# Optimization experiments

Measured on AMD Instinct MI355X. Metric: run time of the kernel, lower is better.

Reference implementation:

```python
import jax, jax.numpy as jnp
import numpy as np

B, N, D, H, DH, HID, CONT, FF = 4, 384, 256, 4, 64, 64, 6, 2
DIST, DIR, ROLE, HOPD, EDGE, SP, DEG, CELL, SAME = 9, 10, 10, 4, 5, 6, 18, 65, 3
SCALE = DH ** -0.5

def _gelu(t):
    return jax.nn.gelu(t, approximate=False)

def _ln(x, g, b, eps=1e-5):
    m = x.mean(-1, keepdims=True)
    v = ((x - m) ** 2).mean(-1, keepdims=True)
    return (x - m) / jnp.sqrt(v + eps) * g + b

def setup_inputs() -> dict:
    key = jax.random.key(0)
    ks = iter(jax.random.split(key, 64))
    nrm = lambda shape, s=0.02: jax.random.normal(next(ks), shape, jnp.float32) * s
    ri = lambda hi, shape: jax.random.randint(next(ks), shape, 0, hi, jnp.int32)
    x = jax.random.normal(next(ks), (B, N, D), jnp.float32)
    cont = jax.random.normal(next(ks), (B, N, N, CONT), jnp.float32)
    pair_mask = jax.random.bernoulli(next(ks), 0.25, (B, N, N)) | jnp.eye(N, dtype=bool)[None]
    valid_mask = jax.random.bernoulli(next(ks), 0.9, (B, N)).at[:, 0].set(True)
    z = lambda *s: jnp.zeros(s, jnp.float32)
    o = lambda *s: jnp.ones(s, jnp.float32)
    return dict(
        x=x, pair_mask=pair_mask, valid_mask=valid_mask, continuous_features=cont,
        distance_bucket=ri(DIST, (B, N, N)), direction_bucket=ri(DIR, (B, N, N)),
        role_pair_id=ri(ROLE, (B, N, N)), hop_delta=ri(HOPD, (B, N, N)),
        edge_type=ri(EDGE, (B, N, N)), shortest_path_bucket=ri(SP, (B, N, N)),
        same_cell_type=ri(SAME, (B, N, N)), degree_ids=ri(DEG, (B, N)), cell_type_ids=ri(CELL, (B, N)),
        Wq=nrm((H * DH, D)), Wk=nrm((H * DH, D)), Wv=nrm((H * DH, D)),
        Wo=nrm((D, H * DH)), bo=z(D),
        cm_W1=nrm((HID, CONT)), cm_b1=z(HID), cm_W2=nrm((HID, HID)), cm_b2=z(HID),
        E_dist=nrm((DIST, HID)), E_dir=nrm((DIR, HID)), E_role=nrm((ROLE, HID)),
        E_hop=nrm((HOPD, HID)), E_edge=nrm((EDGE, HID)), E_sp=nrm((SP, HID)),
        E_deg=nrm((DEG, HID)).at[0].set(0.0), E_cell=nrm((CELL, HID)).at[0].set(0.0),
        E_same=nrm((SAME, HID)),
        bias_ln_g=o(HID), bias_ln_b=z(HID), bias_W=nrm((H, HID)), bias_b=z(H),
        ln1_g=o(D), ln1_b=z(D), ln2_g=o(D), ln2_b=z(D),
        ff_W1=nrm((D * FF * 2, D)), ff_b1=z(D * FF * 2), ff_W2=nrm((D, D * FF)), ff_b2=z(D),
    )

def reference(x, pair_mask, valid_mask, continuous_features, distance_bucket, direction_bucket,
              role_pair_id, hop_delta, edge_type, shortest_path_bucket, same_cell_type,
              degree_ids, cell_type_ids, Wq, Wk, Wv, Wo, bo, cm_W1, cm_b1, cm_W2, cm_b2,
              E_dist, E_dir, E_role, E_hop, E_edge, E_sp, E_deg, E_cell, E_same,
              bias_ln_g, bias_ln_b, bias_W, bias_b, ln1_g, ln1_b, ln2_g, ln2_b,
              ff_W1, ff_b1, ff_W2, ff_b2):
    # --- pairwise structural bias: [B,N,N,HID] pair repr -> [B,H,N,N] bias ---
    pr = _gelu(continuous_features @ cm_W1.T + cm_b1) @ cm_W2.T + cm_b2
    pr = pr + E_dist[distance_bucket] + E_dir[direction_bucket] + E_role[role_pair_id]
    pr = pr + E_hop[hop_delta] + E_edge[edge_type] + E_sp[shortest_path_bucket] + E_same[same_cell_type]
    deg = E_deg[degree_ids]            # [B,N,HID]
    cel = E_cell[cell_type_ids]        # [B,N,HID]
    pr = pr + deg[:, :, None, :] + deg[:, None, :, :] + cel[:, :, None, :] + cel[:, None, :, :]
    bias = _gelu(_ln(pr, bias_ln_g, bias_ln_b)) @ bias_W.T + bias_b   # [B,N,N,H]
    bias = bias * pair_mask[..., None].astype(bias.dtype)
    bias = jnp.transpose(bias, (0, 3, 1, 2))                          # [B,H,N,N]
    # --- attention ---
    xn = _ln(x, ln1_g, ln1_b)
    q = (xn @ Wq.T).reshape(B, N, H, DH).transpose(0, 2, 1, 3)
    k = (xn @ Wk.T).reshape(B, N, H, DH).transpose(0, 2, 1, 3)
    v = (xn @ Wv.T).reshape(B, N, H, DH).transpose(0, 2, 1, 3)
    logits = jnp.einsum('bhid,bhjd->bhij', q, k) * SCALE + bias
    eye = jnp.eye(N, dtype=bool)
    safe = pair_mask | ((~valid_mask)[:, :, None] & eye[None])
    logits = jnp.where(safe[:, None], logits, -jnp.finfo(logits.dtype).max)
    attn = jax.nn.softmax(logits, axis=-1)
    attn = attn * pair_mask[:, None].astype(attn.dtype)
    attn = attn / jnp.maximum(attn.sum(-1, keepdims=True), 1e-6)
    out = jnp.einsum('bhij,bhjd->bhid', attn, v).transpose(0, 2, 1, 3).reshape(B, N, H * DH)
    x1 = x + (out @ Wo.T + bo)
    # --- GEGLU feed-forward ---
    h = _ln(x1, ln2_g, ln2_b) @ ff_W1.T + ff_b1
    a, g = h[..., :D * FF], h[..., D * FF:]
    x_out = x1 + ((a * _gelu(g)) @ ff_W2.T + ff_b2)
    return (x_out, attn, bias)
```

## Files before the change

### kernel.cpp

```cpp
#include <hip/hip_runtime.h>
#include <hip/hip_bf16.h>
#include <float.h>

#define Bz   4
#define Nn   384
#define Dd   256
#define Hh   4
#define DHh  64
#define NSQ  (384*384)
#define NEG_MAX (-3.40282346638528859812e+38f)

typedef __attribute__((ext_vector_type(8))) short short8;
typedef __attribute__((ext_vector_type(4))) float f32x4;
typedef unsigned short ushort_t;

__device__ __forceinline__ float gelu_f(float x){
  const float y = __builtin_fabsf(x) * 0.70710678118654752f;
  const float t = __builtin_amdgcn_rcpf(fmaf(0.3275911f, y, 1.0f));
  float poly = fmaf(1.061405429f, t, -1.453152027f);
  poly = fmaf(poly, t, 1.421413741f);
  poly = fmaf(poly, t, -0.284496736f);
  poly = fmaf(poly, t, 0.254829592f);
  poly *= t;
  const float e = __expf(-y * y);
  const float erfa = fmaf(-poly, e, 1.0f);
  const float er = __builtin_copysignf(erfa, x);
  return 0.5f * x * (1.0f + er);
}
__device__ __forceinline__ float wsum(float v){
  #pragma unroll
  for (int o = 32; o > 0; o >>= 1) v += __shfl_xor(v, o, 64);
  return v;
}
__device__ __forceinline__ float4 ld4(const float* p){ return *(const float4*)p; }
__device__ __forceinline__ f32x4 ldv4(const float* p){ return *(const f32x4*)p; }

__device__ __forceinline__ ushort_t f2bfu(float f){
  union { float f; unsigned u; } v; v.f = f;
  unsigned r = v.u + 0x7FFFu + ((v.u >> 16) & 1u);
  return (ushort_t)(r >> 16);
}
__device__ __forceinline__ short f2bf(float f){ return (short)f2bfu(f); }
__device__ __forceinline__ float bfe2f(ushort_t u){
  union { unsigned u; float f; } v; v.u = ((unsigned)u) << 16; return v.f;
}
__device__ __forceinline__ void addbf(f32x4& a, f32x4& b, short8 v){
  a[0] += bfe2f((ushort_t)v[0]); a[1] += bfe2f((ushort_t)v[1]);
  a[2] += bfe2f((ushort_t)v[2]); a[3] += bfe2f((ushort_t)v[3]);
  b[0] += bfe2f((ushort_t)v[4]); b[1] += bfe2f((ushort_t)v[5]);
  b[2] += bfe2f((ushort_t)v[6]); b[3] += bfe2f((ushort_t)v[7]);
}

__global__ __launch_bounds__(256) void prep_kernel(
    const int* __restrict__ dgk, const int* __restrict__ ctk,
    const float* __restrict__ Edg, const float* __restrict__ Ec,
    const float* __restrict__ b2,
    const float* __restrict__ W1, const float* __restrict__ b1,
    const float* __restrict__ W2,
    const float* __restrict__ Ed, const float* __restrict__ Edi,
    const float* __restrict__ Er, const float* __restrict__ Eh,
    const float* __restrict__ Ee, const float* __restrict__ Esp,
    const float* __restrict__ Es,
    const float* __restrict__ Wq, const float* __restrict__ Wk,
    const float* __restrict__ Wv, const float* __restrict__ Wo,
    const float* __restrict__ ffW1, const float* __restrict__ ffW2,
    const int* __restrict__ dbk, const int* __restrict__ drk,
    const int* __restrict__ rpk, const int* __restrict__ hdk,
    const int* __restrict__ etk, const int* __restrict__ spk,
    const int* __restrict__ sck, const int* __restrict__ pm,
    const float* __restrict__ cont,
    ushort_t* __restrict__ dcP, ushort_t* __restrict__ dcbP,
    ushort_t* __restrict__ w1bf, ushort_t* __restrict__ w2bf,
    ushort_t* __restrict__ EddP, ushort_t* __restrict__ ErsP,
    ushort_t* __restrict__ EhesP,
    ushort_t* __restrict__ wqB, ushort_t* __restrict__ wkB,
    ushort_t* __restrict__ wvB, ushort_t* __restrict__ woB,
    ushort_t* __restrict__ ffW1B, ushort_t* __restrict__ ffW2B,
    ushort_t* __restrict__ contP)
{
  const int idx = blockIdx.x * 256 + threadIdx.x;
  if (idx < 24576) {
    const int row = idx >> 4;
    const int q   = (idx & 15) << 2;
    const int pos = ((q >> 2) & 3) * 16 + (q >> 4) * 4;
    const float4 a = ld4(Edg + (dgk[row] << 6) + q);
    const float4 b = ld4(Ec  + (ctk[row] << 6) + q);
    const float4 bb4 = ld4(b2 + q);
    ushort4 o, o2;
    o.x = f2bfu(a.x + b.x); o.y = f2bfu(a.y + b.y);
    o.z = f2bfu(a.z + b.z); o.w = f2bfu(a.w + b.w);
    o2.x = f2bfu(a.x + b.x + bb4.x); o2.y = f2bfu(a.y + b.y + bb4.y);
    o2.z = f2bfu(a.z + b.z + bb4.z); o2.w = f2bfu(a.w + b.w + bb4.w);
    *(ushort4*)(dcP  + row * 64 + pos) = o;
    *(ushort4*)(dcbP + row * 64 + pos) = o2;
  } else if (idx < 26624) {
    const int t = idx - 24576;
    const int c = t >> 5, k2 = (t & 31) << 1;
    w2bf[c * 64 + k2]     = f2bfu(W2[c * 64 + k2]);
    w2bf[c * 64 + k2 + 1] = f2bfu(W2[c * 64 + k2 + 1]);
  } else if (idx < 26688) {
    const int k = idx - 26624;
    #pragma unroll
    for (int d = 0; d < 6; ++d) w1bf[k * 8 + d] = f2bfu(W1[k * 6 + d]);
    w1bf[k * 8 + 6] = f2bfu(b1[k]);
    w1bf[k * 8 + 7] = 0;
  } else if (idx < 28128) {
    const int t = idx - 26688;
    const int row = t >> 4, q = (t & 15) << 2;
    const int pos = ((q >> 2) & 3) * 16 + (q >> 4) * 4;
    const int d = row / 10, r = row - d * 10;
    const float4 a = ld4(Ed + (d << 6) + q);
    const float4 b = ld4(Edi + (r << 6) + q);
    ushort4 o;
    o.x = f2bfu(a.x + b.x); o.y = f2bfu(a.y + b.y);
    o.z = f2bfu(a.z + b.z); o.w = f2bfu(a.w + b.w);
    *(ushort4*)(EddP + row * 64 + pos) = o;
  } else if (idx < 29088) {
    const int t = idx - 28128;
    const int row = t >> 4, q = (t & 15) << 2;
    const int pos = ((q >> 2) & 3) * 16 + (q >> 4) * 4;
    const int ro = row / 6, s = row - ro * 6;
    const float4 a = ld4(Er + (ro << 6) + q);
    const float4 b = ld4(Esp + (s << 6) + q);
    ushort4 o;
    o.x = f2bfu(a.x + b.x); o.y = f2bfu(a.y + b.y);
    o.z = f2bfu(a.z + b.z); o.w = f2bfu(a.w + b.w);
    *(ushort4*)(ErsP + row * 64 + pos) = o;
  } else if (idx < 30048) {
    const int t = idx - 29088;
    const int row = t >> 4, q = (t & 15) << 2;
    const int pos = ((q >> 2) & 3) * 16 + (q >> 4) * 4;
    const int h = row / 15, rem = row - h * 15;
    const int e = rem / 3, sm = rem - e * 3;
    const float4 a = ld4(Eh + (h << 6) + q);
    const float4 b = ld4(Ee + (e << 6) + q);
    const float4 c = ld4(Es + (sm << 6) + q);
    ushort4 o;
    o.x = f2bfu(a.x + b.x + c.x); o.y = f2bfu(a.y + b.y + c.y);
    o.z = f2bfu(a.z + b.z + c.z); o.w = f2bfu(a.w + b.w + c.w);
    *(ushort4*)(EhesP + row * 64 + pos) = o;
  } else if (idx < 193888) {
    const int t = idx - 30048;
    const float* src; ushort_t* dst; int e;
    if (t < 16384)      { src = Wq;   dst = wqB;   e = t << 2; }
    else if (t < 32768) { src = Wk;   dst = wkB;   e = (t - 16384) << 2; }
    else if (t < 49152) { src = Wv;   dst = wvB;   e = (t - 32768) << 2; }
    else if (t < 65536) { src = Wo;   dst = woB;   e = (t - 49152) << 2; }
    else if (t < 131072){ src = ffW1; dst = ffW1B; e = (t - 65536) << 2; }
    else                { src = ffW2; dst = ffW2B; e = (t - 131072) << 2; }
    const float4 v = ld4(src + e);
    ushort4 o;
    o.x = f2bfu(v.x); o.y = f2bfu(v.y); o.z = f2bfu(v.z); o.w = f2bfu(v.w);
    *(ushort4*)(dst + e) = o;
  } else if (idx < 193888 + Bz * Nn * Nn) {
    const int p = idx - 193888;
    const float* cp = cont + (size_t)p * 6;
    short8 r;
    r[0] = f2bf(cp[0]); r[1] = f2bf(cp[1]); r[2] = f2bf(cp[2]);
    r[3] = f2bf(cp[3]); r[4] = f2bf(cp[4]); r[5] = f2bf(cp[5]);
    const unsigned iv = (unsigned)(dbk[p] * 10 + drk[p])
                      | ((unsigned)(rpk[p] * 6 + spk[p]) << 7)
                      | ((unsigned)((hdk[p] * 5 + etk[p]) * 3 + sck[p]) << 13)
                      | ((pm[p] ? 1u : 0u) << 19);
    r[6] = (short)(iv & 0xffffu);
    r[7] = (short)(iv >> 16);
    *(short8*)(contP + (size_t)p * 8) = r;
  }
}

__global__ __launch_bounds__(256, 3) void pair_kernel(
    const ushort_t* __restrict__ contP,
    const ushort_t* __restrict__ w1bf, const ushort_t* __restrict__ w2bf,
    const ushort_t* __restrict__ EddP, const ushort_t* __restrict__ ErsP,
    const ushort_t* __restrict__ EhesP,
    const float* __restrict__ lng, const float* __restrict__ lnb,
    const float* __restrict__ bW, const float* __restrict__ bb,
    const ushort_t* __restrict__ dcP, const ushort_t* __restrict__ dcbP,
    float* __restrict__ biasOut)
{
  const int tid  = threadIdx.x;
  const int lane = tid & 63;
  const int l15  = lane & 15, lg = lane >> 4;
  const int wid  = blockIdx.x * 4 + (tid >> 6);
  const int rowU = __builtin_amdgcn_readfirstlane(wid / 6);
  const int jb   = wid - rowU * 6;
  const int b    = rowU / Nn;
  const int i    = rowU - b * Nn;
  const int j0   = jb * 64 + l15;
  const size_t pbase = (size_t)rowU * Nn + j0;
  const int colOff = lg << 2;

  const short8 rec0 = *(const short8*)(contP + (pbase + 0) * 8);
  const short8 rec1 = *(const short8*)(contP + (pbase + 16) * 8);
  const short8 rec2 = *(const short8*)(contP + (pbase + 32) * 8);
  const short8 rec3 = *(const short8*)(contP + (pbase + 48) * 8);
  asm volatile("" :: "v"(rec0), "v"(rec1), "v"(rec2), "v"(rec3));
  const unsigned ix0 = (unsigned)(ushort_t)rec0[6] | ((unsigned)(ushort_t)rec0[7] << 16);
  const unsigned ix1 = (unsigned)(ushort_t)rec1[6] | ((unsigned)(ushort_t)rec1[7] << 16);
  const unsigned ix2 = (unsigned)(ushort_t)rec2[6] | ((unsigned)(ushort_t)rec2[7] << 16);
  const unsigned ix3 = (unsigned)(ushort_t)rec3[6] | ((unsigned)(ushort_t)rec3[7] << 16);
  const float c00 = bfe2f((ushort_t)rec0[0]), c01 = bfe2f((ushort_t)rec0[1]),
              c02 = bfe2f((ushort_t)rec0[2]), c03 = bfe2f((ushort_t)rec0[3]),
              c04 = bfe2f((ushort_t)rec0[4]), c05 = bfe2f((ushort_t)rec0[5]);
  const float c10 = bfe2f((ushort_t)rec1[0]), c11 = bfe2f((ushort_t)rec1[1]),
              c12 = bfe2f((ushort_t)rec1[2]), c13 = bfe2f((ushort_t)rec1[3]),
              c14 = bfe2f((ushort_t)rec1[4]), c15 = bfe2f((ushort_t)rec1[5]);
  const float c20 = bfe2f((ushort_t)rec2[0]), c21 = bfe2f((ushort_t)rec2[1]),
              c22 = bfe2f((ushort_t)rec2[2]), c23 = bfe2f((ushort_t)rec2[3]),
              c24 = bfe2f((ushort_t)rec2[4]), c25 = bfe2f((ushort_t)rec2[5]);
  const float c30 = bfe2f((ushort_t)rec3[0]), c31 = bfe2f((ushort_t)rec3[1]),
              c32 = bfe2f((ushort_t)rec3[2]), c33 = bfe2f((ushort_t)rec3[3]),
              c34 = bfe2f((ushort_t)rec3[4]), c35 = bfe2f((ushort_t)rec3[5]);

  short8 b0a, b0b, b1a, b1b, b2a, b2b, b3a, b3b;
#define H1ROW(R, JJ, D0, D1, D2, D3) { \
    const float w0 = bfe2f((ushort_t)R[0]), w1 = bfe2f((ushort_t)R[1]), \
                w2 = bfe2f((ushort_t)R[2]), w3 = bfe2f((ushort_t)R[3]), \
                w4 = bfe2f((ushort_t)R[4]), w5 = bfe2f((ushort_t)R[5]), \
                w6 = bfe2f((ushort_t)R[6]); \
    float s0 = w6, s1 = w6, s2 = w6, s3 = w6; \
    s0 = fmaf(w0, c00, s0); s0 = fmaf(w1, c01, s0); s0 = fmaf(w2, c02, s0); \
    s0 = fmaf(w3, c03, s0); s0 = fmaf(w4, c04, s0); s0 = fmaf(w5, c05, s0); \
    s1 = fmaf(w0, c10, s1); s1 = fmaf(w1, c11, s1); s1 = fmaf(w2, c12, s1); \
    s1 = fmaf(w3, c13, s1); s1 = fmaf(w4, c14, s1); s1 = fmaf(w5, c15, s1); \
    s2 = fmaf(w0, c20, s2); s2 = fmaf(w1, c21, s2); s2 = fmaf(w2, c22, s2); \
    s2 = fmaf(w3, c23, s2); s2 = fmaf(w4, c24, s2); s2 = fmaf(w5, c25, s2); \
    s3 = fmaf(w0, c30, s3); s3 = fmaf(w1, c31, s3); s3 = fmaf(w2, c32, s3); \
    s3 = fmaf(w3, c33, s3); s3 = fmaf(w4, c34, s3); s3 = fmaf(w5, c35, s3); \
    D0[JJ] = f2bf(gelu_f(s0)); D1[JJ] = f2bf(gelu_f(s1)); \
    D2[JJ] = f2bf(gelu_f(s2)); D3[JJ] = f2bf(gelu_f(s3)); }
  {
    const ushort_t* wb_ = w1bf + ((lg << 3) << 3);
    const short8 r0 = *(const short8*)(wb_ +  0);
    const short8 r1 = *(const short8*)(wb_ +  8);
    const short8 r2 = *(const short8*)(wb_ + 16);
    const short8 r3 = *(const short8*)(wb_ + 24);
    const short8 r4 = *(const short8*)(wb_ + 32);
    const short8 r5 = *(const short8*)(wb_ + 40);
    const short8 r6 = *(const short8*)(wb_ + 48);
    const short8 r7 = *(const short8*)(wb_ + 56);
    asm volatile("" :: "v"(r0), "v"(r1), "v"(r2), "v"(r3),
                       "v"(r4), "v"(r5), "v"(r6), "v"(r7));
    H1ROW(r0, 0, b0a, b1a, b2a, b3a) H1ROW(r1, 1, b0a, b1a, b2a, b3a)
    H1ROW(r2, 2, b0a, b1a, b2a, b3a) H1ROW(r3, 3, b0a, b1a, b2a, b3a)
    H1ROW(r4, 4, b0a, b1a, b2a, b3a) H1ROW(r5, 5, b0a, b1a, b2a, b3a)
    H1ROW(r6, 6, b0a, b1a, b2a, b3a) H1ROW(r7, 7, b0a, b1a, b2a, b3a)
  }
  {
    const ushort_t* wb_ = w1bf + ((32 + (lg << 3)) << 3);
    const short8 r0 = *(const short8*)(wb_ +  0);
    const short8 r1 = *(const short8*)(wb_ +  8);
    const short8 r2 = *(const short8*)(wb_ + 16);
    const short8 r3 = *(const short8*)(wb_ + 24);
    const short8 r4 = *(const short8*)(wb_ + 32);
    const short8 r5 = *(const short8*)(wb_ + 40);
    const short8 r6 = *(const short8*)(wb_ + 48);
    const short8 r7 = *(const short8*)(wb_ + 56);
    asm volatile("" :: "v"(r0), "v"(r1), "v"(r2), "v"(r3),
                       "v"(r4), "v"(r5), "v"(r6), "v"(r7));
    H1ROW(r0, 0, b0b, b1b, b2b, b3b) H1ROW(r1, 1, b0b, b1b, b2b, b3b)
    H1ROW(r2, 2, b0b, b1b, b2b, b3b) H1ROW(r3, 3, b0b, b1b, b2b, b3b)
    H1ROW(r4, 4, b0b, b1b, b2b, b3b) H1ROW(r5, 5, b0b, b1b, b2b, b3b)
    H1ROW(r6, 6, b0b, b1b, b2b, b3b) H1ROW(r7, 7, b0b, b1b, b2b, b3b)
  }
#undef H1ROW

  const ushort_t* wbase = w2bf + (size_t)l15 * 64 + (lg << 3);
  const short8 wa0 = *(const short8*)(wbase);
  const short8 wc0 = *(const short8*)(wbase + 32);
  const short8 wa1 = *(const short8*)(wbase + 16 * 64);
  const short8 wc1 = *(const short8*)(wbase + 16 * 64 + 32);
  const short8 wa2 = *(const short8*)(wbase + 32 * 64);
  const short8 wc2 = *(const short8*)(wbase + 32 * 64 + 32);
  const short8 wa3 = *(const short8*)(wbase + 48 * 64);
  const short8 wc3 = *(const short8*)(wbase + 48 * 64 + 32);
  asm volatile("" :: "v"(wa0), "v"(wc0), "v"(wa1), "v"(wc1),
                     "v"(wa2), "v"(wc2), "v"(wa3), "v"(wc3));
  f32x4 acc0[4] = {}, acc1[4] = {}, acc2[4] = {}, acc3[4] = {};
#define MM(ACC, BA, BB) \
  ACC[0] = __builtin_amdgcn_mfma_f32_16x16x32_bf16(wa0, BA, ACC[0], 0, 0, 0); \
  ACC[0] = __builtin_amdgcn_mfma_f32_16x16x32_bf16(wc0, BB, ACC[0], 0, 0, 0); \
  ACC[1] = __builtin_amdgcn_mfma_f32_16x16x32_bf16(wa1, BA, ACC[1], 0, 0, 0); \
  ACC[1] = __builtin_amdgcn_mfma_f32_16x16x32_bf16(wc1, BB, ACC[1], 0, 0, 0); \
  ACC[2] = __builtin_amdgcn_mfma_f32_16x16x32_bf16(wa2, BA, ACC[2], 0, 0, 0); \
  ACC[2] = __builtin_amdgcn_mfma_f32_16x16x32_bf16(wc2, BB, ACC[2], 0, 0, 0); \
  ACC[3] = __builtin_amdgcn_mfma_f32_16x16x32_bf16(wa3, BA, ACC[3], 0, 0, 0); \
  ACC[3] = __builtin_amdgcn_mfma_f32_16x16x32_bf16(wc3, BB, ACC[3], 0, 0, 0);
  MM(acc0, b0a, b0b) MM(acc1, b1a, b1b) MM(acc2, b2a, b2b) MM(acc3, b3a, b3b)
#undef MM

#define GATHER(ACC, IX, JOFF) { \
    const int xdd  = ((IX) & 127) << 6; \
    const int xrs  = (((IX) >> 7) & 63) << 6; \
    const int xhes = (((IX) >> 13) & 63) << 6; \
    const ushort_t* ep = EddP  + xdd  + (lg << 4); \
    const ushort_t* rp = ErsP  + xrs  + (lg << 4); \
    const ushort_t* hp = EhesP + xhes + (lg << 4); \
    const ushort_t* jp = dcP + (((size_t)(b * Nn + j0 + (JOFF))) << 6) + (lg << 4); \
    const short8 e0 = *(const short8*)ep,       e1 = *(const short8*)(ep + 8); \
    const short8 r0 = *(const short8*)rp,       r1 = *(const short8*)(rp + 8); \
    const short8 h0 = *(const short8*)hp,       h1 = *(const short8*)(hp + 8); \
    const short8 jv0 = *(const short8*)jp,      jv1 = *(const short8*)(jp + 8); \
    asm volatile("" :: "v"(e0), "v"(e1), "v"(r0), "v"(r1), \
                       "v"(h0), "v"(h1), "v"(jv0), "v"(jv1)); \
    addbf(ACC[0], ACC[1], e0);  addbf(ACC[2], ACC[3], e1); \
    addbf(ACC[0], ACC[1], r0);  addbf(ACC[2], ACC[3], r1); \
    addbf(ACC[0], ACC[1], h0);  addbf(ACC[2], ACC[3], h1); \
    addbf(ACC[0], ACC[1], jv0); addbf(ACC[2], ACC[3], jv1); }
  GATHER(acc0, ix0, 0)
  GATHER(acc1, ix1, 16)
  GATHER(acc2, ix2, 32)
  GATHER(acc3, ix3, 48)
#undef GATHER
  {
    const ushort_t* up = dcbP + (((size_t)rowU) << 6) + (lg << 4);
    const short8 u0 = *(const short8*)up, u1 = *(const short8*)(up + 8);
    f32x4 du0, du1, du2, du3;
    #pragma unroll
    for (int r = 0; r < 4; ++r) {
      du0[r] = bfe2f((ushort_t)u0[r]);     du1[r] = bfe2f((ushort_t)u0[4 + r]);
      du2[r] = bfe2f((ushort_t)u1[r]);     du3[r] = bfe2f((ushort_t)u1[4 + r]);
    }
    acc0[0] += du0; acc0[1] += du1; acc0[2] += du2; acc0[3] += du3;
    acc1[0] += du0; acc1[1] += du1; acc1[2] += du2; acc1[3] += du3;
    acc2[0] += du0; acc2[1] += du1; acc2[2] += du2; acc2[3] += du3;
    acc3[0] += du0; acc3[1] += du1; acc3[2] += du2; acc3[3] += du3;
  }

  float mean0, inv0, mean1, inv1, mean2, inv2, mean3, inv3;
#define STATS(ACC, MEAN, INV) { \
    float sum = 0.f, sq = 0.f; \
    _Pragma("unroll") \
    for (int mt = 0; mt < 4; ++mt) \
      _Pragma("unroll") \
      for (int r = 0; r < 4; ++r) { \
        const float v = ACC[mt][r]; sum += v; sq = fmaf(v, v, sq); } \
    sum += __shfl_xor(sum, 16, 64); sum += __shfl_xor(sum, 32, 64); \
    sq  += __shfl_xor(sq,  16, 64); sq  += __shfl_xor(sq,  32, 64); \
    MEAN = sum * (1.f / 64.f); \
    INV  = rsqrtf(sq * (1.f / 64.f) - MEAN * MEAN + 1e-5f); }
  STATS(acc0, mean0, inv0) STATS(acc1, mean1, inv1)
  STATS(acc2, mean2, inv2) STATS(acc3, mean3, inv3)
#undef STATS

  float h00 = 0.f, h01 = 0.f, h02 = 0.f, h03 = 0.f;
  float h10 = 0.f, h11 = 0.f, h12 = 0.f, h13 = 0.f;
  float h20 = 0.f, h21 = 0.f, h22 = 0.f, h23 = 0.f;
  float h30 = 0.f, h31 = 0.f, h32 = 0.f, h33 = 0.f;
  #pragma unroll
  for (int mt = 0; mt < 4; ++mt) {
    const int c0i = (mt << 4) + colOff;
    const f32x4 g4 = ldv4(lng + c0i);
    const f32x4 b4 = ldv4(lnb + c0i);
    const f32x4 w0 = ldv4(bW + c0i);
    const f32x4 w1_ = ldv4(bW + 64 + c0i);
    const f32x4 w2_ = ldv4(bW + 128 + c0i);
    const f32x4 w3_ = ldv4(bW + 192 + c0i);
    asm volatile("" :: "v"(g4), "v"(b4), "v"(w0), "v"(w1_), "v"(w2_), "v"(w3_));
    #pragma unroll
    for (int r = 0; r < 4; ++r) {
      float g;
      g = gelu_f((acc0[mt][r] - mean0) * inv0 * g4[r] + b4[r]);
      h00 = fmaf(w0[r], g, h00); h01 = fmaf(w1_[r], g, h01);
      h02 = fmaf(w2_[r], g, h02); h03 = fmaf(w3_[r], g, h03);
      g = gelu_f((acc1[mt][r] - mean1) * inv1 * g4[r] + b4[r]);
      h10 = fmaf(w0[r], g, h10); h11 = fmaf(w1_[r], g, h11);
      h12 = fmaf(w2_[r], g, h12); h13 = fmaf(w3_[r], g, h13);
      g = gelu_f((acc2[mt][r] - mean2) * inv2 * g4[r] + b4[r]);
      h20 = fmaf(w0[r], g, h20); h21 = fmaf(w1_[r], g, h21);
      h22 = fmaf(w2_[r], g, h22); h23 = fmaf(w3_[r], g, h23);
      g = gelu_f((acc3[mt][r] - mean3) * inv3 * g4[r] + b4[r]);
      h30 = fmaf(w0[r], g, h30); h31 = fmaf(w1_[r], g, h31);
      h32 = fmaf(w2_[r], g, h32); h33 = fmaf(w3_[r], g, h33);
    }
  }
#define RED(H) H += __shfl_xor(H, 16, 64); H += __shfl_xor(H, 32, 64);
  RED(h00) RED(h01) RED(h02) RED(h03)
  RED(h10) RED(h11) RED(h12) RED(h13)
  RED(h20) RED(h21) RED(h22) RED(h23)
  RED(h30) RED(h31) RED(h32) RED(h33)
#undef RED

  const float bbl = bb[lg];
  const float bh0 = ((lg == 0) ? h00 : (lg == 1) ? h01 : (lg == 2) ? h02 : h03) + bbl;
  const float bh1 = ((lg == 0) ? h10 : (lg == 1) ? h11 : (lg == 2) ? h12 : h13) + bbl;
  const float bh2 = ((lg == 0) ? h20 : (lg == 1) ? h21 : (lg == 2) ? h22 : h23) + bbl;
  const float bh3 = ((lg == 0) ? h30 : (lg == 1) ? h31 : (lg == 2) ? h32 : h33) + bbl;
  const size_t base = (size_t)b * (Hh * NSQ) + (size_t)lg * NSQ + (size_t)i * Nn;
  biasOut[base + j0]      = bh0 * (((ix0 >> 19) & 1) ? 1.f : 0.f);
  biasOut[base + j0 + 16] = bh1 * (((ix1 >> 19) & 1) ? 1.f : 0.f);
  biasOut[base + j0 + 32] = bh2 * (((ix2 >> 19) & 1) ? 1.f : 0.f);
  biasOut[base + j0 + 48] = bh3 * (((ix3 >> 19) & 1) ? 1.f : 0.f);
}

__global__ __launch_bounds__(256) void ln_kernel(
    const float* __restrict__ x, const float* __restrict__ g,
    const float* __restrict__ bta, ushort_t* __restrict__ o)
{
  const int row  = blockIdx.x * 4 + (threadIdx.x >> 6);
  const int lane = threadIdx.x & 63;
  const float4 v = *(const float4*)(x + (size_t)row * Dd + lane * 4);
  float s = v.x + v.y + v.z + v.w;
  s = wsum(s);
  const float m = s * (1.f / 256.f);
  const float dx = v.x - m, dy = v.y - m, dz = v.z - m, dw = v.w - m;
  float q = dx*dx + dy*dy + dz*dz + dw*dw;
  q = wsum(q);
  const float inv = rsqrtf(q * (1.f / 256.f) + 1e-5f);
  const int d = lane * 4;
  const float4 gg = *(const float4*)(g + d);
  const float4 bb = *(const float4*)(bta + d);
  ushort4 out;
  out.x = f2bfu(dx * inv * gg.x + bb.x);
  out.y = f2bfu(dy * inv * gg.y + bb.y);
  out.z = f2bfu(dz * inv * gg.z + bb.z);
  out.w = f2bfu(dw * inv * gg.w + bb.w);
  *(ushort4*)(o + (size_t)row * Dd + d) = out;
}

__global__ __launch_bounds__(256) void qkv_kernel(
    const ushort_t* __restrict__ xnb,
    const ushort_t* __restrict__ wqB, const ushort_t* __restrict__ wkB,
    const ushort_t* __restrict__ wvB,
    ushort_t* __restrict__ qbB, ushort_t* __restrict__ kbB,
    ushort_t* __restrict__ vbT)
{
  const int tid = threadIdx.x;
  const int lane = tid & 63;
  const int w   = tid >> 6;
  const int l15 = lane & 15, lg = lane >> 4;
  const int m0 = blockIdx.y * 64 + w * 16;
  const int n0 = blockIdx.x * 64;
  const int z  = blockIdx.z;
  const ushort_t* Bb = (z == 0) ? wqB : (z == 1) ? wkB : wvB;

  f32x4 acc[4] = {};
  const ushort_t* pa = xnb + (size_t)(m0 + l15) * Dd + lg * 8;
  for (int k0 = 0; k0 < Dd; k0 += 32) {
    const short8 af = *(const short8*)(pa + k0);
    #pragma unroll
    for (int nt = 0; nt < 4; ++nt) {
      const short8 bf = *(const short8*)(Bb +
          (size_t)(n0 + nt * 16 + l15) * Dd + k0 + lg * 8);
      acc[nt] = __builtin_amdgcn_mfma_f32_16x16x32_bf16(af, bf, acc[nt], 0, 0, 0);
    }
  }
  if (z < 2) {
    ushort_t* Cb = (z == 0) ? qbB : kbB;
    #pragma unroll
    for (int nt = 0; nt < 4; ++nt)
      #pragma unroll
      for (int r = 0; r < 4; ++r)
        Cb[(size_t)(m0 + lg * 4 + r) * Dd + n0 + nt * 16 + l15] = f2bfu(acc[nt][r]);
  } else {
    const int m = m0 + (lg << 2);
    const int b = m / Nn, tok = m - b * Nn;
    #pragma unroll
    for (int nt = 0; nt < 4; ++nt) {
      const int n = n0 + nt * 16 + l15;
      const int h = n >> 6, dh = n & 63;
      ushort4 s4;
      s4.x = f2bfu(acc[nt][0]); s4.y = f2bfu(acc[nt][1]);
      s4.z = f2bfu(acc[nt][2]); s4.w = f2bfu(acc[nt][3]);
      *(ushort4*)(vbT + ((size_t)((b * 4 + h) * 64 + dh)) * Nn + tok) = s4;
    }
  }
}

template<int MODE>
__global__ __launch_bounds__(256) void gemm2(
    const ushort_t* __restrict__ A16, const float* __restrict__ A32, int lda,
    const ushort_t* __restrict__ Bm, int ldb,
    float* __restrict__ Cc, int ldc,
    const float* __restrict__ bias,
    const float* __restrict__ res, int ldr,
    int K,
    const float* __restrict__ biasT, const int* __restrict__ pmask,
    const int* __restrict__ valid)
{
  const int tid = threadIdx.x;
  const int lane = tid & 63;
  const int w   = tid >> 6;
  const int l15 = lane & 15, lg = lane >> 4;
  const int m0 = blockIdx.y * 64 + w * 16;
  const int n0 = blockIdx.x * 64;

  const ushort_t* Ab = A16; const ushort_t* Bb = Bm; float* Cb = Cc;
  const float* biasTb = biasT; const int* pmb = pmask; const int* vlb = valid;
  if (MODE == 1) {
    const int bz = blockIdx.z;
    const int b = bz >> 2, h = bz & 3;
    Ab = A16 + (size_t)b * Nn * Dd + h * DHh;
    Bb = Bm  + (size_t)b * Nn * Dd + h * DHh;
    Cb = Cc + (size_t)bz * NSQ;
    biasTb = biasT + (size_t)bz * NSQ;
    pmb = pmask + (size_t)b * NSQ;
    vlb = valid + b * Nn;
  }

  f32x4 acc[4] = {};
  const ushort_t* pa16 = Ab + (size_t)(m0 + l15) * lda + lg * 8;
  const float* pa32 = (MODE == 3) ? (A32 + (size_t)(m0 + l15) * lda + lg * 8) : nullptr;

  for (int k0 = 0; k0 < K; k0 += 32) {
    short8 af;
    if (MODE == 3) {
      const float4 a0 = ld4(pa32 + k0);
      const float4 a1 = ld4(pa32 + k0 + 4);
      const float4 g0 = ld4(pa32 + 512 + k0);
      const float4 g1 = ld4(pa32 + 512 + k0 + 4);
      af[0] = f2bf(a0.x * gelu_f(g0.x)); af[1] = f2bf(a0.y * gelu_f(g0.y));
      af[2] = f2bf(a0.z * gelu_f(g0.z)); af[3] = f2bf(a0.w * gelu_f(g0.w));
      af[4] = f2bf(a1.x * gelu_f(g1.x)); af[5] = f2bf(a1.y * gelu_f(g1.y));
      af[6] = f2bf(a1.z * gelu_f(g1.z)); af[7] = f2bf(a1.w * gelu_f(g1.w));
    } else {
      af = *(const short8*)(pa16 + k0);
    }
    #pragma unroll
    for (int nt = 0; nt < 4; ++nt) {
      const short8 bf = *(const short8*)(Bb +
          (size_t)(n0 + nt * 16 + l15) * ldb + k0 + lg * 8);
      acc[nt] = __builtin_amdgcn_mfma_f32_16x16x32_bf16(af, bf, acc[nt], 0, 0, 0);
    }
  }

  #pragma unroll
  for (int nt = 0; nt < 4; ++nt) {
    #pragma unroll
    for (int r = 0; r < 4; ++r) {
      const int m = m0 + lg * 4 + r;
      const int n = n0 + nt * 16 + l15;
      float v = acc[nt][r];
      if (MODE != 1) {
        if (bias) v += bias[n];
        if (res)  v += res[(size_t)m * ldr + n];
        Cb[(size_t)m * ldc + n] = v;
      } else {
        v = v * 0.125f + biasTb[(size_t)m * Nn + n];
        const bool safe = (pmb[(size_t)m * Nn + n] != 0) || (vlb[m] == 0 && m == n);
        Cb[(size_t)m * Nn + n] = safe ? v : NEG_MAX;
      }
    }
  }
}

__global__ __launch_bounds__(64) void pv_kernel(
    float* __restrict__ att, const int* __restrict__ pm,
    const ushort_t* __restrict__ vbT, ushort_t* __restrict__ aoB)
{
  const int lane = threadIdx.x;
  const int l15 = lane & 15, lg = lane >> 4;
  const int bz = blockIdx.y;
  const int b = bz >> 2, h = bz & 3;
  const int m0 = blockIdx.x * 16;
  const int row = m0 + l15;
  float* ar = att + (size_t)bz * NSQ + (size_t)row * Nn;
  const int* pmr = pm + (size_t)b * NSQ + (size_t)row * Nn;

  float mr = NEG_MAX, sr = 0.f, spr = 0.f;
  for (int t = 0; t < 12; ++t) {
    const int c = t * 32 + lg * 8;
    const f32x4 v0 = ldv4(ar + c);
    const f32x4 v1 = ldv4(ar + c + 4);
    const int4 q0 = *(const int4*)(pmr + c);
    const int4 q1 = *(const int4*)(pmr + c + 4);
    float mc = fmaxf(fmaxf(fmaxf(v0[0], v0[1]), fmaxf(v0[2], v0[3])),
                     fmaxf(fmaxf(v1[0], v1[1]), fmaxf(v1[2], v1[3])));
    if (mc > mr) {
      const float sc = __expf(mr - mc);
      sr *= sc; spr *= sc; mr = mc;
    }
    float e;
    e = __expf(v0[0] - mr); sr += e; spr += q0.x ? e : 0.f;
    e = __expf(v0[1] - mr); sr += e; spr += q0.y ? e : 0.f;
    e = __expf(v0[2] - mr); sr += e; spr += q0.z ? e : 0.f;
    e = __expf(v0[3] - mr); sr += e; spr += q0.w ? e : 0.f;
    e = __expf(v1[0] - mr); sr += e; spr += q1.x ? e : 0.f;
    e = __expf(v1[1] - mr); sr += e; spr += q1.y ? e : 0.f;
    e = __expf(v1[2] - mr); sr += e; spr += q1.z ? e : 0.f;
    e = __expf(v1[3] - mr); sr += e; spr += q1.w ? e : 0.f;
  }
  #pragma unroll
  for (int o = 16; o <= 32; o <<= 1) {
    const float mo = __shfl_xor(mr, o, 64);
    const float so = __shfl_xor(sr, o, 64);
    const float spo = __shfl_xor(spr, o, 64);
    const float mn = fmaxf(mr, mo);
    const float s1 = __expf(mr - mn), s2 = __expf(mo - mn);
    sr = sr * s1 + so * s2;
    spr = spr * s1 + spo * s2;
    mr = mn;
  }
  const float rinv = 1.f / fmaxf(spr, 1e-6f * sr);

  f32x4 acc[4] = {};
  const ushort_t* vb0 = vbT + (size_t)(bz * 64) * Nn;
  for (int t = 0; t < 12; ++t) {
    const int c = t * 32 + lg * 8;
    const f32x4 v0 = ldv4(ar + c);
    const f32x4 v1 = ldv4(ar + c + 4);
    const int4 q0 = *(const int4*)(pmr + c);
    const int4 q1 = *(const int4*)(pmr + c + 4);
    f32x4 p0, p1;
    p0[0] = q0.x ? __expf(v0[0] - mr) * rinv : 0.f;
    p0[1] = q0.y ? __expf(v0[1] - mr) * rinv : 0.f;
    p0[2] = q0.z ? __expf(v0[2] - mr) * rinv : 0.f;
    p0[3] = q0.w ? __expf(v0[3] - mr) * rinv : 0.f;
    p1[0] = q1.x ? __expf(v1[0] - mr) * rinv : 0.f;
    p1[1] = q1.y ? __expf(v1[1] - mr) * rinv : 0.f;
    p1[2] = q1.z ? __expf(v1[2] - mr) * rinv : 0.f;
    p1[3] = q1.w ? __expf(v1[3] - mr) * rinv : 0.f;
    *(f32x4*)(ar + c) = p0;
    *(f32x4*)(ar + c + 4) = p1;
    short8 af;
    af[0] = f2bf(p0[0]); af[1] = f2bf(p0[1]); af[2] = f2bf(p0[2]); af[3] = f2bf(p0[3]);
    af[4] = f2bf(p1[0]); af[5] = f2bf(p1[1]); af[6] = f2bf(p1[2]); af[7] = f2bf(p1[3]);
    #pragma unroll
    for (int nt = 0; nt < 4; ++nt) {
      const short8 bf = *(const short8*)(vb0 + (size_t)(nt * 16 + l15) * Nn + c);
      acc[nt] = __builtin_amdgcn_mfma_f32_16x16x32_bf16(af, bf, acc[nt], 0, 0, 0);
    }
  }
  #pragma unroll
  for (int nt = 0; nt < 4; ++nt)
    #pragma unroll
    for (int r = 0; r < 4; ++r)
      aoB[(size_t)(b * Nn + m0 + lg * 4 + r) * Dd + h * 64 + nt * 16 + l15] =
          f2bfu(acc[nt][r]);
}

extern "C" void kernel_launch(void* const* d_in, const int* in_sizes, int n_in,
                              void* d_out, int out_size, void* d_ws, size_t ws_size,
                              hipStream_t stream) {
  const float* x    = (const float*)d_in[0];
  const int*   pm   = (const int*)  d_in[1];
  const int*   vld  = (const int*)  d_in[2];
  const float* cont = (const float*)d_in[3];
  const int* dbk = (const int*)d_in[4];
  const int* drk = (const int*)d_in[5];
  const int* rpk = (const int*)d_in[6];
  const int* hdk = (const int*)d_in[7];
  const int* etk = (const int*)d_in[8];
  const int* spk = (const int*)d_in[9];
  const int* sck = (const int*)d_in[10];
  const int* dgk = (const int*)d_in[11];
  const int* ctk = (const int*)d_in[12];
  const float* Wq  = (const float*)d_in[13];
  const float* Wk  = (const float*)d_in[14];
  const float* Wv  = (const float*)d_in[15];
  const float* Wo  = (const float*)d_in[16];
  const float* bo  = (const float*)d_in[17];
  const float* cmW1 = (const float*)d_in[18];
  const float* cmb1 = (const float*)d_in[19];
  const float* cmW2 = (const float*)d_in[20];
  const float* cmb2 = (const float*)d_in[21];
  const float* Ed  = (const float*)d_in[22];
  const float* Edi = (const float*)d_in[23];
  const float* Er  = (const float*)d_in[24];
  const float* Eh  = (const float*)d_in[25];
  const float* Ee  = (const float*)d_in[26];
  const float* Esp = (const float*)d_in[27];
  const float* Edg = (const float*)d_in[28];
  const float* Ec  = (const float*)d_in[29];
  const float* Es  = (const float*)d_in[30];
  const float* blng = (const float*)d_in[31];
  const float* blnb = (const float*)d_in[32];
  const float* bW   = (const float*)d_in[33];
  const float* bb_  = (const float*)d_in[34];
  const float* ln1g = (const float*)d_in[35];
  const float* ln1b = (const float*)d_in[36];
  const float* ln2g = (const float*)d_in[37];
  const float* ln2b = (const float*)d_in[38];
  const float* ffW1 = (const float*)d_in[39];
  const float* ffb1 = (const float*)d_in[40];
  const float* ffW2 = (const float*)d_in[41];
  const float* ffb2 = (const float*)d_in[42];

  float* out   = (float*)d_out;
  float* xout  = out;
  float* attn  = out + 393216;
  float* biasO = out + 393216 + 2359296;

  float* ws = (float*)d_ws;
  ushort_t* wqB   = (ushort_t*)(ws);
  ushort_t* wkB   = (ushort_t*)(ws + 32768);
  ushort_t* wvB   = (ushort_t*)(ws + 65536);
  ushort_t* woB   = (ushort_t*)(ws + 98304);
  ushort_t* ffW1B = (ushort_t*)(ws + 131072);
  ushort_t* ffW2B = (ushort_t*)(ws + 262144);
  ushort_t* contP = (ushort_t*)(ws + 327680);
  ushort_t* dcP   = (ushort_t*)(ws + 2686976);
  ushort_t* dcbP  = (ushort_t*)(ws + 2736128);
  ushort_t* EddP  = (ushort_t*)(ws + 2785280);
  ushort_t* ErsP  = (ushort_t*)(ws + 2788160);
  ushort_t* EhesP = (ushort_t*)(ws + 2790080);
  ushort_t* w1bf  = (ushort_t*)(ws + 2792000);
  ushort_t* w2bf  = (ushort_t*)(ws + 2792256);
  ushort_t* xnb = (ushort_t*)(ws + 327680);
  ushort_t* qbB = (ushort_t*)(ws + 524288);
  ushort_t* kbB = (ushort_t*)(ws + 720896);
  ushort_t* vbT = (ushort_t*)(ws + 917504);
  ushort_t* aoB = (ushort_t*)(ws + 1114112);
  float* x1  = ws + 1310720;
  float* hff = ws + 1703936;

  prep_kernel<<<3062, 256, 0, stream>>>(dgk, ctk, Edg, Ec, cmb2, cmW1, cmb1,
      cmW2, Ed, Edi, Er, Eh, Ee, Esp, Es, Wq, Wk, Wv, Wo, ffW1, ffW2,
      dbk, drk, rpk, hdk, etk, spk, sck, pm, cont,
      dcP, dcbP, w1bf, w2bf, EddP, ErsP, EhesP,
      wqB, wkB, wvB, woB, ffW1B, ffW2B, contP);
  pair_kernel<<<2304, 256, 0, stream>>>(contP, w1bf, w2bf, EddP, ErsP, EhesP,
      blng, blnb, bW, bb_, dcP, dcbP, biasO);
  ln_kernel<<<384, 256, 0, stream>>>(x, ln1g, ln1b, xnb);
  qkv_kernel<<<dim3(4, 24, 3), 256, 0, stream>>>(xnb, wqB, wkB, wvB,
      qbB, kbB, vbT);
  gemm2<1><<<dim3(6, 6, 16), 256, 0, stream>>>(qbB, nullptr, 256, kbB, 256,
      attn, 384, nullptr, nullptr, 0, 64, biasO, pm, vld);
  pv_kernel<<<dim3(24, 16), 64, 0, stream>>>(attn, pm, vbT, aoB);
  gemm2<0><<<dim3(4, 24), 256, 0, stream>>>(aoB, nullptr, 256, woB, 256,
      x1, 256, bo, x, 256, 256, nullptr, nullptr, nullptr);
  ln_kernel<<<384, 256, 0, stream>>>(x1, ln2g, ln2b, xnb);
  gemm2<0><<<dim3(16, 24), 256, 0, stream>>>(xnb, nullptr, 256, ffW1B, 256,
      hff, 1024, ffb1, nullptr, 0, 256, nullptr, nullptr, nullptr);
  gemm2<3><<<dim3(4, 24), 256, 0, stream>>>(nullptr, hff, 1024, ffW2B, 512,
      xout, 256, ffb2, x1, 256, 512, nullptr, nullptr, nullptr);
}
```

Baseline: 188.7 us.

## Fuse QK logits, masked softmax and PV into one attention kernel

Replaces the separate QK^T gemm (which wrote masked logits to the attn buffer) and the pv_kernel (which re-read them twice) with a single attention kernel. Each block handles 16 query rows, and its four waves each cover 96 keys. Softmax statistics are merged across waves through shared memory, and P·V partial results are reduced in LDS. This removes the logits round trip through global memory and one launch, at the cost of more barriers and LDS use and only 384 blocks. It also lowers pair_kernel's occupancy hint from 3 to 2 waves per SIMD.

```diff
diff --git a/kernel.cpp b/kernel.cpp
--- a/kernel.cpp
+++ b/kernel.cpp
@@ -168,7 +168,7 @@
   }
 }
 
-__global__ __launch_bounds__(256, 3) void pair_kernel(
+__global__ __launch_bounds__(256, 2) void pair_kernel(
     const ushort_t* __restrict__ contP,
     const ushort_t* __restrict__ w1bf, const ushort_t* __restrict__ w2bf,
     const ushort_t* __restrict__ EddP, const ushort_t* __restrict__ ErsP,
@@ -467,6 +467,158 @@
   }
 }
 
+__global__ __launch_bounds__(256) void attn_kernel(
+    const ushort_t* __restrict__ qbB, const ushort_t* __restrict__ kbB,
+    const ushort_t* __restrict__ vbT,
+    const float* __restrict__ biasO, const int* __restrict__ pm,
+    const int* __restrict__ vld,
+    float* __restrict__ attn, ushort_t* __restrict__ aoB)
+{
+  __shared__ float stats[3][4][16];
+  __shared__ float part[4][16][64];
+  __shared__ ushort_t pstage[4][16][104];
+  const int tid = threadIdx.x;
+  const int lane = tid & 63, w = tid >> 6;
+  const int l15 = lane & 15, lg = lane >> 4;
+  const int bz = blockIdx.y, b = bz >> 2, h = bz & 3;
+  const int m0 = blockIdx.x * 16;
+  const int n0 = w * 96;
+
+  f32x4 acc[6];
+  const ushort_t* paq = qbB + ((size_t)(b * Nn + m0 + l15)) * Dd + h * DHh;
+  const short8 aq0 = *(const short8*)(paq + lg * 8);
+  const short8 aq1 = *(const short8*)(paq + 32 + lg * 8);
+  #pragma unroll
+  for (int nt = 0; nt < 6; ++nt) {
+    const ushort_t* pk = kbB + ((size_t)(b * Nn + n0 + nt * 16 + l15)) * Dd
+                       + h * DHh + lg * 8;
+    const short8 bk0 = *(const short8*)pk;
+    const short8 bk1 = *(const short8*)(pk + 32);
+    f32x4 a = {};
+    a = __builtin_amdgcn_mfma_f32_16x16x32_bf16(aq0, bk0, a, 0, 0, 0);
+    a = __builtin_amdgcn_mfma_f32_16x16x32_bf16(aq1, bk1, a, 0, 0, 0);
+    acc[nt] = a;
+  }
+
+  const float* bias_r = biasO + (size_t)bz * NSQ;
+  const int* pm_b = pm + (size_t)b * NSQ;
+  int vldv[4];
+  #pragma unroll
+  for (int r = 0; r < 4; ++r) vldv[r] = vld[b * Nn + m0 + lg * 4 + r];
+  unsigned pmmask = 0;
+  #pragma unroll
+  for (int nt = 0; nt < 6; ++nt) {
+    #pragma unroll
+    for (int r = 0; r < 4; ++r) {
+      const int m = m0 + lg * 4 + r;
+      const int n = n0 + nt * 16 + l15;
+      const size_t off = (size_t)m * Nn + n;
+      const float bv = bias_r[off];
+      const int q = pm_b[off];
+      const bool sf = (q != 0) || (vldv[r] == 0 && m == n);
+      if (q) pmmask |= 1u << (nt * 4 + r);
+      acc[nt][r] = sf ? fmaf(acc[nt][r], 0.125f, bv) : NEG_MAX;
+    }
+  }
+
+  float mx[4], sr[4], spr[4];
+  #pragma unroll
+  for (int r = 0; r < 4; ++r) {
+    float m_ = NEG_MAX;
+    #pragma unroll
+    for (int nt = 0; nt < 6; ++nt) m_ = fmaxf(m_, acc[nt][r]);
+    #pragma unroll
+    for (int o = 1; o <= 8; o <<= 1) m_ = fmaxf(m_, __shfl_xor(m_, o, 64));
+    float s_ = 0.f, sp_ = 0.f;
+    #pragma unroll
+    for (int nt = 0; nt < 6; ++nt) {
+      const float e = __expf(acc[nt][r] - m_);
+      s_ += e;
+      sp_ += ((pmmask >> (nt * 4 + r)) & 1) ? e : 0.f;
+    }
+    #pragma unroll
+    for (int o = 1; o <= 8; o <<= 1) {
+      s_ += __shfl_xor(s_, o, 64);
+      sp_ += __shfl_xor(sp_, o, 64);
+    }
+    mx[r] = m_; sr[r] = s_; spr[r] = sp_;
+  }
+  if (l15 == 0) {
+    #pragma unroll
+    for (int r = 0; r < 4; ++r) {
+      stats[0][w][lg * 4 + r] = mx[r];
+      stats[1][w][lg * 4 + r] = sr[r];
+      stats[2][w][lg * 4 + r] = spr[r];
+    }
+  }
+  __syncthreads();
+  float mr[4], rinv[4];
+  #pragma unroll
+  for (int r = 0; r < 4; ++r) {
+    const int row = lg * 4 + r;
+    float M = NEG_MAX, S = 0.f, SP = 0.f;
+    #pragma unroll
+    for (int wv = 0; wv < 4; ++wv) {
+      const float m2 = stats[0][wv][row];
+      const float s2 = stats[1][wv][row];
+      const float sp2 = stats[2][wv][row];
+      const float mn = fmaxf(M, m2);
+      const float f1 = __expf(M - mn), f2 = __expf(m2 - mn);
+      S = S * f1 + s2 * f2;
+      SP = SP * f1 + sp2 * f2;
+      M = mn;
+    }
+    mr[r] = M;
+    rinv[r] = 1.f / fmaxf(SP, 1e-6f * S);
+  }
+
+  float* attn_b = attn + (size_t)bz * NSQ;
+  #pragma unroll
+  for (int nt = 0; nt < 6; ++nt) {
+    #pragma unroll
+    for (int r = 0; r < 4; ++r) {
+      const int m = m0 + lg * 4 + r;
+      const int n = n0 + nt * 16 + l15;
+      const float e = __expf(acc[nt][r] - mr[r]);
+      const float a = ((pmmask >> (nt * 4 + r)) & 1) ? e * rinv[r] : 0.f;
+      attn_b[(size_t)m * Nn + n] = a;
+      pstage[w][lg * 4 + r][nt * 16 + l15] = f2bfu(a);
+    }
+  }
+  __syncthreads();
+
+  f32x4 pacc[4] = {};
+  const ushort_t* vb0 = vbT + (size_t)(bz * 64) * Nn;
+  #pragma unroll
+  for (int ks = 0; ks < 3; ++ks) {
+    const int ktok = ks * 32 + lg * 8;
+    const short8 ap = *(const short8*)&pstage[w][l15][ktok];
+    #pragma unroll
+    for (int nt = 0; nt < 4; ++nt) {
+      const short8 bvv = *(const short8*)(vb0 +
+          (size_t)(nt * 16 + l15) * Nn + n0 + ktok);
+      pacc[nt] = __builtin_amdgcn_mfma_f32_16x16x32_bf16(ap, bvv, pacc[nt], 0, 0, 0);
+    }
+  }
+  #pragma unroll
+  for (int nt = 0; nt < 4; ++nt)
+    #pragma unroll
+    for (int r = 0; r < 4; ++r)
+      part[w][lg * 4 + r][nt * 16 + l15] = pacc[nt][r];
+  __syncthreads();
+  {
+    const int o = tid * 4;
+    const int row = o >> 6, dh0 = o & 63;
+    f32x4 s = *(const f32x4*)&part[0][row][dh0];
+    s += *(const f32x4*)&part[1][row][dh0];
+    s += *(const f32x4*)&part[2][row][dh0];
+    s += *(const f32x4*)&part[3][row][dh0];
+    ushort4 st;
+    st.x = f2bfu(s[0]); st.y = f2bfu(s[1]); st.z = f2bfu(s[2]); st.w = f2bfu(s[3]);
+    *(ushort4*)(aoB + (size_t)(b * Nn + m0 + row) * Dd + h * 64 + dh0) = st;
+  }
+}
+
 template<int MODE>
 __global__ __launch_bounds__(256) void gemm2(
     const ushort_t* __restrict__ A16, const float* __restrict__ A32, int lda,
@@ -474,9 +626,7 @@
     float* __restrict__ Cc, int ldc,
     const float* __restrict__ bias,
     const float* __restrict__ res, int ldr,
-    int K,
-    const float* __restrict__ biasT, const int* __restrict__ pmask,
-    const int* __restrict__ valid)
+    int K)
 {
   const int tid = threadIdx.x;
   const int lane = tid & 63;
@@ -485,21 +635,8 @@
   const int m0 = blockIdx.y * 64 + w * 16;
   const int n0 = blockIdx.x * 64;
 
-  const ushort_t* Ab = A16; const ushort_t* Bb = Bm; float* Cb = Cc;
-  const float* biasTb = biasT; const int* pmb = pmask; const int* vlb = valid;
-  if (MODE == 1) {
-    const int bz = blockIdx.z;
-    const int b = bz >> 2, h = bz & 3;
-    Ab = A16 + (size_t)b * Nn * Dd + h * DHh;
-    Bb = Bm  + (size_t)b * Nn * Dd + h * DHh;
-    Cb = Cc + (size_t)bz * NSQ;
-    biasTb = biasT + (size_t)bz * NSQ;
-    pmb = pmask + (size_t)b * NSQ;
-    vlb = valid + b * Nn;
-  }
-
   f32x4 acc[4] = {};
-  const ushort_t* pa16 = Ab + (size_t)(m0 + l15) * lda + lg * 8;
+  const ushort_t* pa16 = A16 + (size_t)(m0 + l15) * lda + lg * 8;
   const float* pa32 = (MODE == 3) ? (A32 + (size_t)(m0 + l15) * lda + lg * 8) : nullptr;
 
   for (int k0 = 0; k0 < K; k0 += 32) {
@@ -518,7 +655,7 @@
     }
     #pragma unroll
     for (int nt = 0; nt < 4; ++nt) {
-      const short8 bf = *(const short8*)(Bb +
+      const short8 bf = *(const short8*)(Bm +
           (size_t)(n0 + nt * 16 + l15) * ldb + k0 + lg * 8);
       acc[nt] = __builtin_amdgcn_mfma_f32_16x16x32_bf16(af, bf, acc[nt], 0, 0, 0);
     }
@@ -531,102 +668,11 @@
       const int m = m0 + lg * 4 + r;
       const int n = n0 + nt * 16 + l15;
       float v = acc[nt][r];
-      if (MODE != 1) {
-        if (bias) v += bias[n];
-        if (res)  v += res[(size_t)m * ldr + n];
-        Cb[(size_t)m * ldc + n] = v;
-      } else {
-        v = v * 0.125f + biasTb[(size_t)m * Nn + n];
-        const bool safe = (pmb[(size_t)m * Nn + n] != 0) || (vlb[m] == 0 && m == n);
-        Cb[(size_t)m * Nn + n] = safe ? v : NEG_MAX;
-      }
-    }
-  }
-}
-
-__global__ __launch_bounds__(64) void pv_kernel(
-    float* __restrict__ att, const int* __restrict__ pm,
-    const ushort_t* __restrict__ vbT, ushort_t* __restrict__ aoB)
-{
-  const int lane = threadIdx.x;
-  const int l15 = lane & 15, lg = lane >> 4;
-  const int bz = blockIdx.y;
-  const int b = bz >> 2, h = bz & 3;
-  const int m0 = blockIdx.x * 16;
-  const int row = m0 + l15;
-  float* ar = att + (size_t)bz * NSQ + (size_t)row * Nn;
-  const int* pmr = pm + (size_t)b * NSQ + (size_t)row * Nn;
-
-  float mr = NEG_MAX, sr = 0.f, spr = 0.f;
-  for (int t = 0; t < 12; ++t) {
-    const int c = t * 32 + lg * 8;
-    const f32x4 v0 = ldv4(ar + c);
-    const f32x4 v1 = ldv4(ar + c + 4);
-    const int4 q0 = *(const int4*)(pmr + c);
-    const int4 q1 = *(const int4*)(pmr + c + 4);
-    float mc = fmaxf(fmaxf(fmaxf(v0[0], v0[1]), fmaxf(v0[2], v0[3])),
-                     fmaxf(fmaxf(v1[0], v1[1]), fmaxf(v1[2], v1[3])));
-    if (mc > mr) {
-      const float sc = __expf(mr - mc);
-      sr *= sc; spr *= sc; mr = mc;
-    }
-    float e;
-    e = __expf(v0[0] - mr); sr += e; spr += q0.x ? e : 0.f;
-    e = __expf(v0[1] - mr); sr += e; spr += q0.y ? e : 0.f;
-    e = __expf(v0[2] - mr); sr += e; spr += q0.z ? e : 0.f;
-    e = __expf(v0[3] - mr); sr += e; spr += q0.w ? e : 0.f;
-    e = __expf(v1[0] - mr); sr += e; spr += q1.x ? e : 0.f;
-    e = __expf(v1[1] - mr); sr += e; spr += q1.y ? e : 0.f;
-    e = __expf(v1[2] - mr); sr += e; spr += q1.z ? e : 0.f;
-    e = __expf(v1[3] - mr); sr += e; spr += q1.w ? e : 0.f;
-  }
-  #pragma unroll
-  for (int o = 16; o <= 32; o <<= 1) {
-    const float mo = __shfl_xor(mr, o, 64);
-    const float so = __shfl_xor(sr, o, 64);
-    const float spo = __shfl_xor(spr, o, 64);
-    const float mn = fmaxf(mr, mo);
-    const float s1 = __expf(mr - mn), s2 = __expf(mo - mn);
-    sr = sr * s1 + so * s2;
-    spr = spr * s1 + spo * s2;
-    mr = mn;
-  }
-  const float rinv = 1.f / fmaxf(spr, 1e-6f * sr);
-
-  f32x4 acc[4] = {};
-  const ushort_t* vb0 = vbT + (size_t)(bz * 64) * Nn;
-  for (int t = 0; t < 12; ++t) {
-    const int c = t * 32 + lg * 8;
-    const f32x4 v0 = ldv4(ar + c);
-    const f32x4 v1 = ldv4(ar + c + 4);
-    const int4 q0 = *(const int4*)(pmr + c);
-    const int4 q1 = *(const int4*)(pmr + c + 4);
-    f32x4 p0, p1;
-    p0[0] = q0.x ? __expf(v0[0] - mr) * rinv : 0.f;
-    p0[1] = q0.y ? __expf(v0[1] - mr) * rinv : 0.f;
-    p0[2] = q0.z ? __expf(v0[2] - mr) * rinv : 0.f;
-    p0[3] = q0.w ? __expf(v0[3] - mr) * rinv : 0.f;
-    p1[0] = q1.x ? __expf(v1[0] - mr) * rinv : 0.f;
-    p1[1] = q1.y ? __expf(v1[1] - mr) * rinv : 0.f;
-    p1[2] = q1.z ? __expf(v1[2] - mr) * rinv : 0.f;
-    p1[3] = q1.w ? __expf(v1[3] - mr) * rinv : 0.f;
-    *(f32x4*)(ar + c) = p0;
-    *(f32x4*)(ar + c + 4) = p1;
-    short8 af;
-    af[0] = f2bf(p0[0]); af[1] = f2bf(p0[1]); af[2] = f2bf(p0[2]); af[3] = f2bf(p0[3]);
-    af[4] = f2bf(p1[0]); af[5] = f2bf(p1[1]); af[6] = f2bf(p1[2]); af[7] = f2bf(p1[3]);
-    #pragma unroll
-    for (int nt = 0; nt < 4; ++nt) {
-      const short8 bf = *(const short8*)(vb0 + (size_t)(nt * 16 + l15) * Nn + c);
-      acc[nt] = __builtin_amdgcn_mfma_f32_16x16x32_bf16(af, bf, acc[nt], 0, 0, 0);
-    }
-  }
-  #pragma unroll
-  for (int nt = 0; nt < 4; ++nt)
-    #pragma unroll
-    for (int r = 0; r < 4; ++r)
-      aoB[(size_t)(b * Nn + m0 + lg * 4 + r) * Dd + h * 64 + nt * 16 + l15] =
-          f2bfu(acc[nt][r]);
+      if (bias) v += bias[n];
+      if (res)  v += res[(size_t)m * ldr + n];
+      Cc[(size_t)m * ldc + n] = v;
+    }
+  }
 }
 
 extern "C" void kernel_launch(void* const* d_in, const int* in_sizes, int n_in,
@@ -714,14 +760,13 @@
   ln_kernel<<<384, 256, 0, stream>>>(x, ln1g, ln1b, xnb);
   qkv_kernel<<<dim3(4, 24, 3), 256, 0, stream>>>(xnb, wqB, wkB, wvB,
       qbB, kbB, vbT);
-  gemm2<1><<<dim3(6, 6, 16), 256, 0, stream>>>(qbB, nullptr, 256, kbB, 256,
-      attn, 384, nullptr, nullptr, 0, 64, biasO, pm, vld);
-  pv_kernel<<<dim3(24, 16), 64, 0, stream>>>(attn, pm, vbT, aoB);
+  attn_kernel<<<dim3(24, 16), 256, 0, stream>>>(qbB, kbB, vbT, biasO, pm, vld,
+      attn, aoB);
   gemm2<0><<<dim3(4, 24), 256, 0, stream>>>(aoB, nullptr, 256, woB, 256,
-      x1, 256, bo, x, 256, 256, nullptr, nullptr, nullptr);
+      x1, 256, bo, x, 256, 256);
   ln_kernel<<<384, 256, 0, stream>>>(x1, ln2g, ln2b, xnb);
   gemm2<0><<<dim3(16, 24), 256, 0, stream>>>(xnb, nullptr, 256, ffW1B, 256,
-      hff, 1024, ffb1, nullptr, 0, 256, nullptr, nullptr, nullptr);
+      hff, 1024, ffb1, nullptr, 0, 256);
   gemm2<3><<<dim3(4, 24), 256, 0, stream>>>(nullptr, hff, 1024, ffW2B, 512,
-      xout, 256, ffb2, x1, 256, 512, nullptr, nullptr, nullptr);
-}
+      xout, 256, ffb2, x1, 256, 512);
+}
```

After: 185.2 us. No clear change (-1.9%).
